# Kernel tuning notes

Hardware: AMD Instinct MI355X
Metric: run time of the kernel (lower is better)

The kernel has to match this reference:

```python
import jax, jax.numpy as jnp
import numpy as np


def setup_inputs() -> dict:
    key = jax.random.key(0)
    k1, k2 = jax.random.split(key)
    T, D, E = 8192, 4096, 64  # tokens, model_dim, num_experts
    x = jax.random.normal(k1, (T, D), dtype=jnp.float32)
    wg = jax.random.normal(k2, (E, D), dtype=jnp.float32) * (1.0 / np.sqrt(D))
    return {"x": x, "wg": wg}


def reference(x, wg):
    # gate logits: nn.Linear(model_dim, num_experts, bias=False) in fp32
    logits = jnp.einsum('td,ed->te', x.astype(jnp.float32), wg)  # [T, E]
    gates = jax.nn.softmax(logits, axis=1)                        # [T, E]
    # top1gating (eval mode: no noise): argmax over gates
    indices1_s = jnp.argmax(gates, axis=1)                        # [T] int
    # gates = (gates * one_hot(indices1_s)).sum(dim=1) == gather of the max gate
    gates1_s = jnp.take_along_axis(gates, indices1_s[:, None], axis=1)[:, 0]  # [T]
    return indices1_s, gates1_s
```

## Files before the change

kernel.cpp:

```cpp
#include <hip/hip_runtime.h>

typedef __attribute__((ext_vector_type(8))) short bf16x8;
typedef __attribute__((ext_vector_type(4))) float f32x4;

constexpr int TN = 8192;
constexpr int DN = 4096;
constexpr int EN = 64;

constexpr int NS     = DN / 32;
constexpr int KSPLIT = 16;
constexpr int SLOTS  = NS / KSPLIT;
constexpr int RB     = 512;
constexpr int RW     = 64;

__device__ __forceinline__ unsigned short f2bf(float f) {
    unsigned u = __builtin_bit_cast(unsigned, f);
    u += 0x7FFFu + ((u >> 16) & 1u);
    return (unsigned short)(u >> 16);
}
__device__ __forceinline__ float bf2f(unsigned short h) {
    unsigned u = ((unsigned)h) << 16;
    return __builtin_bit_cast(float, u);
}
__device__ __forceinline__ void split_pair(float f0, float f1,
                                           unsigned& hi, unsigned& lo) {
    unsigned u0 = __builtin_bit_cast(unsigned, f0);
    unsigned u1 = __builtin_bit_cast(unsigned, f1);
    unsigned r0 = u0 + 0x7FFFu + ((u0 >> 16) & 1u);
    unsigned r1 = u1 + 0x7FFFu + ((u1 >> 16) & 1u);
    hi = __builtin_amdgcn_perm(r1, r0, 0x07060302u);
    float h0 = __builtin_bit_cast(float, r0 & 0xFFFF0000u);
    float h1 = __builtin_bit_cast(float, r1 & 0xFFFF0000u);
    unsigned v0 = __builtin_bit_cast(unsigned, f0 - h0);
    unsigned v1 = __builtin_bit_cast(unsigned, f1 - h1);
    unsigned s0 = v0 + 0x7FFFu + ((v0 >> 16) & 1u);
    unsigned s1 = v1 + 0x7FFFu + ((v1 >> 16) & 1u);
    lo = __builtin_amdgcn_perm(s1, s0, 0x07060302u);
}

__global__ __launch_bounds__(256)
void wg_frag_kernel(const float* __restrict__ wg, unsigned short* __restrict__ BF) {
    const int gid = blockIdx.x * 256 + threadIdx.x;
    const int l  = gid & 63;
    const int et = (gid >> 6) & 3;
    const int s  = (gid >> 8) & (NS - 1);
    const int p  = gid >> 15;
    const int e  = et * 16 + (l & 15);
    const int k  = s * 32 + (l >> 4) * 8;

    const float* src = wg + (size_t)e * DN + k;
    float4 v0 = *reinterpret_cast<const float4*>(src);
    float4 v1 = *reinterpret_cast<const float4*>(src + 4);
    float f[8] = {v0.x, v0.y, v0.z, v0.w, v1.x, v1.y, v1.z, v1.w};
    unsigned short o[8];
#pragma unroll
    for (int j = 0; j < 8; ++j) {
        unsigned short h = f2bf(f[j]);
        o[j] = p ? f2bf(f[j] - bf2f(h)) : h;
    }
    unsigned short* dst = BF + (((size_t)p * NS + s) * 4 + et) * 512 + (size_t)l * 8;
    *reinterpret_cast<ushort4*>(dst)     = make_ushort4(o[0], o[1], o[2], o[3]);
    *reinterpret_cast<ushort4*>(dst + 4) = make_ushort4(o[4], o[5], o[6], o[7]);
}

__global__ __launch_bounds__(512, 2)
void gate_gemm_kernel(const float* __restrict__ x,
                      const unsigned short* __restrict__ BF,
                      float* __restrict__ part) {
    __shared__ uint4 LB[SLOTS * 512];

    const int tid  = threadIdx.x;
    const int lane = tid & 63;
    const int w    = tid >> 6;
    const int rt   = blockIdx.x >> 4;
    const int ks   = blockIdx.x & 15;
    const int r0   = rt * RB;

    const int fr = lane & 15;
    const int g  = lane >> 4;
    const int fko = g * 8;

    {
        const uint4* gh = reinterpret_cast<const uint4*>(BF);
        const uint4* gl = gh + 32768;
#pragma unroll
        for (int i = 0; i < 8; ++i) {
            int e = tid + i * 512;
            int slot = e >> 9, plane = (e >> 8) & 1, off = e & 255;
            int gidx = (ks * SLOTS + slot) * 256 + off;
            LB[e] = plane ? gl[gidx] : gh[gidx];
        }
    }
    __syncthreads();

    const float* xa = x + (size_t)(r0 + w * RW + fr) * DN + fko;

    f32x4 acc[4][4] = {};
    float4 XA[2][4][2];

    auto loadA = [&](int set, int t) {
        const float* p = xa + (size_t)(ks * SLOTS + t) * 32;
#pragma unroll
        for (int rh = 0; rh < 4; ++rh) {
            const float* pr = p + (size_t)rh * 16 * DN;
            XA[set][rh][0] = *reinterpret_cast<const float4*>(pr);
            XA[set][rh][1] = *reinterpret_cast<const float4*>(pr + 4);
        }
    };
    auto compute = [&](int set, int t) {
        bf16x8 bh[4], bl[4];
#pragma unroll
        for (int et = 0; et < 4; ++et) {
            bh[et] = __builtin_bit_cast(bf16x8, LB[t * 512 + et * 64 + lane]);
            bl[et] = __builtin_bit_cast(bf16x8, LB[t * 512 + 256 + et * 64 + lane]);
        }
        bf16x8 ah[4], al[4];
#pragma unroll
        for (int rh = 0; rh < 4; ++rh) {
            float f[8] = {XA[set][rh][0].x, XA[set][rh][0].y,
                          XA[set][rh][0].z, XA[set][rh][0].w,
                          XA[set][rh][1].x, XA[set][rh][1].y,
                          XA[set][rh][1].z, XA[set][rh][1].w};
            unsigned uh[4], ul[4];
#pragma unroll
            for (int q = 0; q < 4; ++q)
                split_pair(f[2 * q], f[2 * q + 1], uh[q], ul[q]);
            uint4 vh = make_uint4(uh[0], uh[1], uh[2], uh[3]);
            uint4 vl = make_uint4(ul[0], ul[1], ul[2], ul[3]);
            ah[rh] = __builtin_bit_cast(bf16x8, vh);
            al[rh] = __builtin_bit_cast(bf16x8, vl);
        }
#pragma unroll
        for (int et = 0; et < 4; ++et)
#pragma unroll
            for (int rh = 0; rh < 4; ++rh)
                acc[rh][et] = __builtin_amdgcn_mfma_f32_16x16x32_bf16(ah[rh], bh[et], acc[rh][et], 0, 0, 0);
#pragma unroll
        for (int et = 0; et < 4; ++et)
#pragma unroll
            for (int rh = 0; rh < 4; ++rh)
                acc[rh][et] = __builtin_amdgcn_mfma_f32_16x16x32_bf16(al[rh], bh[et], acc[rh][et], 0, 0, 0);
#pragma unroll
        for (int et = 0; et < 4; ++et)
#pragma unroll
            for (int rh = 0; rh < 4; ++rh)
                acc[rh][et] = __builtin_amdgcn_mfma_f32_16x16x32_bf16(ah[rh], bl[et], acc[rh][et], 0, 0, 0);
#pragma unroll
        for (int et = 0; et < 4; ++et)
#pragma unroll
            for (int rh = 0; rh < 4; ++rh)
                acc[rh][et] = __builtin_amdgcn_mfma_f32_16x16x32_bf16(al[rh], bl[et], acc[rh][et], 0, 0, 0);
    };

    loadA(0, 0);
    loadA(1, 1);
#pragma unroll
    for (int t = 0; t < SLOTS; ++t) {
        compute(t & 1, t);
        if (t + 2 < SLOTS) loadA(t & 1, t + 2);
        asm volatile("" ::: "memory");
    }

    float* dst = part + ((size_t)ks * TN + r0 + w * RW) * EN;
#pragma unroll
    for (int rh = 0; rh < 4; ++rh)
#pragma unroll
        for (int et = 0; et < 4; ++et)
#pragma unroll
            for (int r = 0; r < 4; ++r)
                dst[(size_t)(rh * 16 + g * 4 + r) * EN + et * 16 + fr] = acc[rh][et][r];
}

__global__ __launch_bounds__(256)
void top1_softmax_kernel(const float* __restrict__ part, float* __restrict__ out) {
    const int gid = blockIdx.x * blockDim.x + threadIdx.x;
    const int row = gid >> 4;
    const int eg  = gid & 15;
    if (row >= TN) return;

    float v[4] = {};
#pragma unroll
    for (int h = 0; h < KSPLIT; ++h) {
        float4 t = *reinterpret_cast<const float4*>(
            &part[((size_t)h * TN + row) * EN + eg * 4]);
        v[0] += t.x; v[1] += t.y; v[2] += t.z; v[3] += t.w;
    }
    float m = v[0];
    int idx = eg * 4;
#pragma unroll
    for (int j = 1; j < 4; ++j)
        if (v[j] > m) { m = v[j]; idx = eg * 4 + j; }
#pragma unroll
    for (int d = 1; d < 16; d <<= 1) {
        float om = __shfl_xor(m, d);
        int   oi = __shfl_xor(idx, d);
        if (om > m || (om == m && oi < idx)) { m = om; idx = oi; }
    }
    float s = 0.0f;
#pragma unroll
    for (int j = 0; j < 4; ++j) s += __expf(v[j] - m);
#pragma unroll
    for (int d = 1; d < 16; d <<= 1) s += __shfl_xor(s, d);
    if (eg == 0) {
        out[row]      = (float)idx;
        out[TN + row] = 1.0f / s;
    }
}

extern "C" void kernel_launch(void* const* d_in, const int* in_sizes, int n_in,
                              void* d_out, int out_size, void* d_ws, size_t ws_size,
                              hipStream_t stream) {
    const float* x  = (const float*)d_in[0];
    const float* wg = (const float*)d_in[1];
    float* out = (float*)d_out;

    constexpr size_t BF_BYTES = (size_t)2 * NS * 4 * 512 * 2;
    unsigned short* BF = (unsigned short*)d_ws;
    float* part = (float*)((char*)d_ws + BF_BYTES);

    wg_frag_kernel<<<dim3(256), dim3(256), 0, stream>>>(wg, BF);
    gate_gemm_kernel<<<dim3((TN / RB) * KSPLIT), dim3(512), 0, stream>>>(x, BF, part);
    top1_softmax_kernel<<<dim3(TN * 16 / 256), dim3(256), 0, stream>>>(part, out);
}
```

Measured before the change: 42.75 us.

## Shrink per-wave row tile and drop low-by-low MFMA correction term

Each wave now computes 16 rows instead of 64, so blocks cover 128 rows and the grid grows fourfold, with launch bounds asking for more resident blocks. The split-bf16 product also drops the al*bl term, using three MFMA passes instead of four. The aim is better latency hiding and load balance in this x-bandwidth-bound GEMM, plus less MFMA and register work. In exchange, each block still fills its full 64KB LDS slice of the weights, so weight staging traffic per row rises. Dropping the smallest correction term slightly reduces precision.

```diff
diff --git a/kernel.cpp b/kernel.cpp
--- a/kernel.cpp
+++ b/kernel.cpp
@@ -10,8 +10,8 @@
 constexpr int NS     = DN / 32;
 constexpr int KSPLIT = 16;
 constexpr int SLOTS  = NS / KSPLIT;
-constexpr int RB     = 512;
-constexpr int RW     = 64;
+constexpr int RB     = 128;
+constexpr int RW     = 16;
 
 __device__ __forceinline__ unsigned short f2bf(float f) {
     unsigned u = __builtin_bit_cast(unsigned, f);
@@ -63,7 +63,7 @@
     *reinterpret_cast<ushort4*>(dst + 4) = make_ushort4(o[4], o[5], o[6], o[7]);
 }
 
-__global__ __launch_bounds__(512, 2)
+__global__ __launch_bounds__(512, 4)
 void gate_gemm_kernel(const float* __restrict__ x,
                       const unsigned short* __restrict__ BF,
                       float* __restrict__ part) {
@@ -78,7 +78,6 @@
 
     const int fr = lane & 15;
     const int g  = lane >> 4;
-    const int fko = g * 8;
 
     {
         const uint4* gh = reinterpret_cast<const uint4*>(BF);
@@ -93,19 +92,15 @@
     }
     __syncthreads();
 
-    const float* xa = x + (size_t)(r0 + w * RW + fr) * DN + fko;
-
-    f32x4 acc[4][4] = {};
-    float4 XA[2][4][2];
+    const float* xa = x + (size_t)(r0 + w * RW + fr) * DN + g * 8;
+
+    f32x4 acc[4] = {};
+    float4 XA[2][2];
 
     auto loadA = [&](int set, int t) {
         const float* p = xa + (size_t)(ks * SLOTS + t) * 32;
-#pragma unroll
-        for (int rh = 0; rh < 4; ++rh) {
-            const float* pr = p + (size_t)rh * 16 * DN;
-            XA[set][rh][0] = *reinterpret_cast<const float4*>(pr);
-            XA[set][rh][1] = *reinterpret_cast<const float4*>(pr + 4);
-        }
+        XA[set][0] = *reinterpret_cast<const float4*>(p);
+        XA[set][1] = *reinterpret_cast<const float4*>(p + 4);
     };
     auto compute = [&](int set, int t) {
         bf16x8 bh[4], bl[4];
@@ -114,42 +109,25 @@
             bh[et] = __builtin_bit_cast(bf16x8, LB[t * 512 + et * 64 + lane]);
             bl[et] = __builtin_bit_cast(bf16x8, LB[t * 512 + 256 + et * 64 + lane]);
         }
-        bf16x8 ah[4], al[4];
-#pragma unroll
-        for (int rh = 0; rh < 4; ++rh) {
-            float f[8] = {XA[set][rh][0].x, XA[set][rh][0].y,
-                          XA[set][rh][0].z, XA[set][rh][0].w,
-                          XA[set][rh][1].x, XA[set][rh][1].y,
-                          XA[set][rh][1].z, XA[set][rh][1].w};
-            unsigned uh[4], ul[4];
-#pragma unroll
-            for (int q = 0; q < 4; ++q)
-                split_pair(f[2 * q], f[2 * q + 1], uh[q], ul[q]);
-            uint4 vh = make_uint4(uh[0], uh[1], uh[2], uh[3]);
-            uint4 vl = make_uint4(ul[0], ul[1], ul[2], ul[3]);
-            ah[rh] = __builtin_bit_cast(bf16x8, vh);
-            al[rh] = __builtin_bit_cast(bf16x8, vl);
-        }
+        float f[8] = {XA[set][0].x, XA[set][0].y, XA[set][0].z, XA[set][0].w,
+                      XA[set][1].x, XA[set][1].y, XA[set][1].z, XA[set][1].w};
+        unsigned uh[4], ul[4];
+#pragma unroll
+        for (int q = 0; q < 4; ++q)
+            split_pair(f[2 * q], f[2 * q + 1], uh[q], ul[q]);
+        uint4 vh = make_uint4(uh[0], uh[1], uh[2], uh[3]);
+        uint4 vl = make_uint4(ul[0], ul[1], ul[2], ul[3]);
+        bf16x8 ah = __builtin_bit_cast(bf16x8, vh);
+        bf16x8 al = __builtin_bit_cast(bf16x8, vl);
 #pragma unroll
         for (int et = 0; et < 4; ++et)
-#pragma unroll
-            for (int rh = 0; rh < 4; ++rh)
-                acc[rh][et] = __builtin_amdgcn_mfma_f32_16x16x32_bf16(ah[rh], bh[et], acc[rh][et], 0, 0, 0);
+            acc[et] = __builtin_amdgcn_mfma_f32_16x16x32_bf16(ah, bh[et], acc[et], 0, 0, 0);
 #pragma unroll
         for (int et = 0; et < 4; ++et)
-#pragma unroll
-            for (int rh = 0; rh < 4; ++rh)
-                acc[rh][et] = __builtin_amdgcn_mfma_f32_16x16x32_bf16(al[rh], bh[et], acc[rh][et], 0, 0, 0);
+            acc[et] = __builtin_amdgcn_mfma_f32_16x16x32_bf16(al, bh[et], acc[et], 0, 0, 0);
 #pragma unroll
         for (int et = 0; et < 4; ++et)
-#pragma unroll
-            for (int rh = 0; rh < 4; ++rh)
-                acc[rh][et] = __builtin_amdgcn_mfma_f32_16x16x32_bf16(ah[rh], bl[et], acc[rh][et], 0, 0, 0);
-#pragma unroll
-        for (int et = 0; et < 4; ++et)
-#pragma unroll
-            for (int rh = 0; rh < 4; ++rh)
-                acc[rh][et] = __builtin_amdgcn_mfma_f32_16x16x32_bf16(al[rh], bl[et], acc[rh][et], 0, 0, 0);
+            acc[et] = __builtin_amdgcn_mfma_f32_16x16x32_bf16(ah, bl[et], acc[et], 0, 0, 0);
     };
 
     loadA(0, 0);
@@ -163,12 +141,10 @@
 
     float* dst = part + ((size_t)ks * TN + r0 + w * RW) * EN;
 #pragma unroll
-    for (int rh = 0; rh < 4; ++rh)
-#pragma unroll
-        for (int et = 0; et < 4; ++et)
-#pragma unroll
-            for (int r = 0; r < 4; ++r)
-                dst[(size_t)(rh * 16 + g * 4 + r) * EN + et * 16 + fr] = acc[rh][et][r];
+    for (int et = 0; et < 4; ++et)
+#pragma unroll
+        for (int r = 0; r < 4; ++r)
+            dst[(size_t)(g * 4 + r) * EN + et * 16 + fr] = acc[et][r];
 }
 
 __global__ __launch_bounds__(256)
```

Result: slower. 45.21 us (+5.7%).

## Restructure gate GEMM to intra-block K-split with LDS reduction

Applied to the files above, without the earlier changes.

The GEMM now splits K across the 8 waves of a block, each handling 64 rows, and loads the bf16 weight fragments straight from global memory into registers with double buffering. The separate LDS staging of B and its barrier are gone. Partial sums from the 8 waves are reduced in LDS, so only two K-split partials per row go to global memory instead of sixteen. This cuts partial-sum traffic and lets the softmax kernel become one thread per row, at the cost of redundant B loads per wave and an LDS reduction epilogue.

```diff
diff --git a/kernel.cpp b/kernel.cpp
--- a/kernel.cpp
+++ b/kernel.cpp
@@ -7,11 +7,10 @@
 constexpr int DN = 4096;
 constexpr int EN = 64;
 
-constexpr int NS     = DN / 32;
-constexpr int KSPLIT = 16;
-constexpr int SLOTS  = NS / KSPLIT;
-constexpr int RB     = 512;
-constexpr int RW     = 64;
+constexpr int BM = 64;
+constexpr int NS = DN / 32;
+constexpr int KSPLIT = 2;
+constexpr int NTW = (NS / KSPLIT) / 8;
 
 __device__ __forceinline__ unsigned short f2bf(float f) {
     unsigned u = __builtin_bit_cast(unsigned, f);
@@ -67,39 +66,29 @@
 void gate_gemm_kernel(const float* __restrict__ x,
                       const unsigned short* __restrict__ BF,
                       float* __restrict__ part) {
-    __shared__ uint4 LB[SLOTS * 512];
+    __shared__ float L[4][BM][68];
 
     const int tid  = threadIdx.x;
     const int lane = tid & 63;
     const int w    = tid >> 6;
-    const int rt   = blockIdx.x >> 4;
-    const int ks   = blockIdx.x & 15;
-    const int r0   = rt * RB;
+    const int rt   = blockIdx.x >> 1;
+    const int ks   = blockIdx.x & 1;
+    const int r0   = rt * BM;
+    const int sbase = ks * (NS / KSPLIT);
 
     const int fr = lane & 15;
     const int g  = lane >> 4;
-    const int fko = g * 8;
-
-    {
-        const uint4* gh = reinterpret_cast<const uint4*>(BF);
-        const uint4* gl = gh + 32768;
-#pragma unroll
-        for (int i = 0; i < 8; ++i) {
-            int e = tid + i * 512;
-            int slot = e >> 9, plane = (e >> 8) & 1, off = e & 255;
-            int gidx = (ks * SLOTS + slot) * 256 + off;
-            LB[e] = plane ? gl[gidx] : gh[gidx];
-        }
-    }
-    __syncthreads();
-
-    const float* xa = x + (size_t)(r0 + w * RW + fr) * DN + fko;
+
+    const float* xa = x + (size_t)(r0 + fr) * DN + g * 8;
 
     f32x4 acc[4][4] = {};
+
     float4 XA[2][4][2];
+    bf16x8 Bq[2][8];
 
     auto loadA = [&](int set, int t) {
-        const float* p = xa + (size_t)(ks * SLOTS + t) * 32;
+        const int s = sbase + t * 8 + w;
+        const float* p = xa + (size_t)s * 32;
 #pragma unroll
         for (int rh = 0; rh < 4; ++rh) {
             const float* pr = p + (size_t)rh * 16 * DN;
@@ -107,13 +96,17 @@
             XA[set][rh][1] = *reinterpret_cast<const float4*>(pr + 4);
         }
     };
-    auto compute = [&](int set, int t) {
-        bf16x8 bh[4], bl[4];
-#pragma unroll
-        for (int et = 0; et < 4; ++et) {
-            bh[et] = __builtin_bit_cast(bf16x8, LB[t * 512 + et * 64 + lane]);
-            bl[et] = __builtin_bit_cast(bf16x8, LB[t * 512 + 256 + et * 64 + lane]);
-        }
+    auto loadB = [&](int set, int t) {
+        const int s = sbase + t * 8 + w;
+        const unsigned short* bp = BF + (size_t)s * 2048 + (size_t)lane * 8;
+#pragma unroll
+        for (int et = 0; et < 4; ++et)
+            Bq[set][et] = *reinterpret_cast<const bf16x8*>(bp + et * 512);
+#pragma unroll
+        for (int et = 0; et < 4; ++et)
+            Bq[set][4 + et] = *reinterpret_cast<const bf16x8*>(bp + (size_t)NS * 2048 + et * 512);
+    };
+    auto compute = [&](int set) {
         bf16x8 ah[4], al[4];
 #pragma unroll
         for (int rh = 0; rh < 4; ++rh) {
@@ -134,77 +127,95 @@
         for (int et = 0; et < 4; ++et)
 #pragma unroll
             for (int rh = 0; rh < 4; ++rh)
-                acc[rh][et] = __builtin_amdgcn_mfma_f32_16x16x32_bf16(ah[rh], bh[et], acc[rh][et], 0, 0, 0);
-#pragma unroll
-        for (int et = 0; et < 4; ++et)
-#pragma unroll
-            for (int rh = 0; rh < 4; ++rh)
-                acc[rh][et] = __builtin_amdgcn_mfma_f32_16x16x32_bf16(al[rh], bh[et], acc[rh][et], 0, 0, 0);
-#pragma unroll
-        for (int et = 0; et < 4; ++et)
-#pragma unroll
-            for (int rh = 0; rh < 4; ++rh)
-                acc[rh][et] = __builtin_amdgcn_mfma_f32_16x16x32_bf16(ah[rh], bl[et], acc[rh][et], 0, 0, 0);
-#pragma unroll
-        for (int et = 0; et < 4; ++et)
-#pragma unroll
-            for (int rh = 0; rh < 4; ++rh)
-                acc[rh][et] = __builtin_amdgcn_mfma_f32_16x16x32_bf16(al[rh], bl[et], acc[rh][et], 0, 0, 0);
+                acc[rh][et] = __builtin_amdgcn_mfma_f32_16x16x32_bf16(ah[rh], Bq[set][et], acc[rh][et], 0, 0, 0);
+#pragma unroll
+        for (int et = 0; et < 4; ++et)
+#pragma unroll
+            for (int rh = 0; rh < 4; ++rh)
+                acc[rh][et] = __builtin_amdgcn_mfma_f32_16x16x32_bf16(al[rh], Bq[set][et], acc[rh][et], 0, 0, 0);
+#pragma unroll
+        for (int et = 0; et < 4; ++et)
+#pragma unroll
+            for (int rh = 0; rh < 4; ++rh)
+                acc[rh][et] = __builtin_amdgcn_mfma_f32_16x16x32_bf16(ah[rh], Bq[set][4 + et], acc[rh][et], 0, 0, 0);
+#pragma unroll
+        for (int et = 0; et < 4; ++et)
+#pragma unroll
+            for (int rh = 0; rh < 4; ++rh)
+                acc[rh][et] = __builtin_amdgcn_mfma_f32_16x16x32_bf16(al[rh], Bq[set][4 + et], acc[rh][et], 0, 0, 0);
     };
 
+    loadB(0, 0);
     loadA(0, 0);
+    loadB(1, 1);
     loadA(1, 1);
 #pragma unroll
-    for (int t = 0; t < SLOTS; ++t) {
-        compute(t & 1, t);
-        if (t + 2 < SLOTS) loadA(t & 1, t + 2);
+    for (int t = 0; t < NTW; ++t) {
+        compute(t & 1);
+        if (t + 2 < NTW) { loadB(t & 1, t + 2); loadA(t & 1, t + 2); }
         asm volatile("" ::: "memory");
     }
 
-    float* dst = part + ((size_t)ks * TN + r0 + w * RW) * EN;
-#pragma unroll
-    for (int rh = 0; rh < 4; ++rh)
-#pragma unroll
-        for (int et = 0; et < 4; ++et)
-#pragma unroll
-            for (int r = 0; r < 4; ++r)
-                dst[(size_t)(rh * 16 + g * 4 + r) * EN + et * 16 + fr] = acc[rh][et][r];
+    if (w < 4) {
+#pragma unroll
+        for (int rh = 0; rh < 4; ++rh)
+#pragma unroll
+            for (int et = 0; et < 4; ++et)
+#pragma unroll
+                for (int r = 0; r < 4; ++r)
+                    L[w][rh * 16 + g * 4 + r][et * 16 + fr] = acc[rh][et][r];
+    }
+    __syncthreads();
+    if (w >= 4) {
+#pragma unroll
+        for (int rh = 0; rh < 4; ++rh)
+#pragma unroll
+            for (int et = 0; et < 4; ++et)
+#pragma unroll
+                for (int r = 0; r < 4; ++r)
+                    L[w - 4][rh * 16 + g * 4 + r][et * 16 + fr] += acc[rh][et][r];
+    }
+    __syncthreads();
+
+    {
+        const int row = tid >> 3;
+        const int eg  = tid & 7;
+        float v[8];
+#pragma unroll
+        for (int j = 0; j < 8; ++j)
+            v[j] = L[0][row][eg * 8 + j] + L[1][row][eg * 8 + j]
+                 + L[2][row][eg * 8 + j] + L[3][row][eg * 8 + j];
+        float* dst = part + ((size_t)ks * TN + r0 + row) * EN + eg * 8;
+        *reinterpret_cast<float4*>(dst)     = make_float4(v[0], v[1], v[2], v[3]);
+        *reinterpret_cast<float4*>(dst + 4) = make_float4(v[4], v[5], v[6], v[7]);
+    }
 }
 
 __global__ __launch_bounds__(256)
 void top1_softmax_kernel(const float* __restrict__ part, float* __restrict__ out) {
-    const int gid = blockIdx.x * blockDim.x + threadIdx.x;
-    const int row = gid >> 4;
-    const int eg  = gid & 15;
+    const int row = blockIdx.x * blockDim.x + threadIdx.x;
     if (row >= TN) return;
 
-    float v[4] = {};
-#pragma unroll
-    for (int h = 0; h < KSPLIT; ++h) {
-        float4 t = *reinterpret_cast<const float4*>(
-            &part[((size_t)h * TN + row) * EN + eg * 4]);
-        v[0] += t.x; v[1] += t.y; v[2] += t.z; v[3] += t.w;
-    }
+    float v[EN];
+#pragma unroll
+    for (int i = 0; i < EN / 4; ++i) {
+        float4 s = *reinterpret_cast<const float4*>(&part[(size_t)row * EN + i * 4]);
+        float4 t = *reinterpret_cast<const float4*>(&part[((size_t)TN + row) * EN + i * 4]);
+        v[i * 4 + 0] = s.x + t.x; v[i * 4 + 1] = s.y + t.y;
+        v[i * 4 + 2] = s.z + t.z; v[i * 4 + 3] = s.w + t.w;
+    }
+
     float m = v[0];
-    int idx = eg * 4;
-#pragma unroll
-    for (int j = 1; j < 4; ++j)
-        if (v[j] > m) { m = v[j]; idx = eg * 4 + j; }
-#pragma unroll
-    for (int d = 1; d < 16; d <<= 1) {
-        float om = __shfl_xor(m, d);
-        int   oi = __shfl_xor(idx, d);
-        if (om > m || (om == m && oi < idx)) { m = om; idx = oi; }
-    }
+    int idx = 0;
+#pragma unroll
+    for (int e = 1; e < EN; ++e)
+        if (v[e] > m) { m = v[e]; idx = e; }
     float s = 0.0f;
 #pragma unroll
-    for (int j = 0; j < 4; ++j) s += __expf(v[j] - m);
-#pragma unroll
-    for (int d = 1; d < 16; d <<= 1) s += __shfl_xor(s, d);
-    if (eg == 0) {
-        out[row]      = (float)idx;
-        out[TN + row] = 1.0f / s;
-    }
+    for (int e = 0; e < EN; ++e) s += __expf(v[e] - m);
+
+    out[row]      = (float)idx;
+    out[TN + row] = 1.0f / s;
 }
 
 extern "C" void kernel_launch(void* const* d_in, const int* in_sizes, int n_in,
@@ -219,6 +230,6 @@
     float* part = (float*)((char*)d_ws + BF_BYTES);
 
     wg_frag_kernel<<<dim3(256), dim3(256), 0, stream>>>(wg, BF);
-    gate_gemm_kernel<<<dim3((TN / RB) * KSPLIT), dim3(512), 0, stream>>>(x, BF, part);
-    top1_softmax_kernel<<<dim3(TN * 16 / 256), dim3(256), 0, stream>>>(part, out);
-}
+    gate_gemm_kernel<<<dim3(128 * KSPLIT), dim3(512), 0, stream>>>(x, BF, part);
+    top1_softmax_kernel<<<dim3(TN / 256), dim3(256), 0, stream>>>(part, out);
+}
```

Result: no change. 43.39 us (+1.5%).
